# Optimization experiments

Measured on AMD Instinct MI355X. Metric: run time of the kernel, lower is better.

The kernel has to match this reference:

```python
import jax, jax.numpy as jnp
import numpy as np

EPS = 1e-6
MAX_TANH_ARG = 15.0


def setup_inputs() -> dict:
    key = jax.random.key(0)
    k1, k2, k3 = jax.random.split(key, 3)
    B, H, N, D = 2, 16, 2048, 64
    return {
        "q": jax.random.normal(k1, (B, H, N, D), dtype=jnp.float32),
        "k": jax.random.normal(k2, (B, H, N, D), dtype=jnp.float32),
        "v": jax.random.normal(k3, (B, H, N, D), dtype=jnp.float32),
        "c": jnp.ones((1,), dtype=jnp.float32),
        "beta": jnp.ones((1,), dtype=jnp.float32),
    }


def _exp_map(x, sqrt_c):
    # tangent space -> Poincare ball
    norm = jnp.maximum(jnp.linalg.norm(x, axis=-1, keepdims=True), EPS)
    tanh_arg = jnp.minimum(sqrt_c * norm, MAX_TANH_ARG)
    return x * (jnp.tanh(tanh_arg) / (sqrt_c * norm))


def reference(q, k, v, c, beta):
    # q, k, v: [B, H, N, D]; c, beta: [1] positive scalars
    causal, use_exp_map = True, True
    N = q.shape[2]
    c = jnp.maximum(c.astype(jnp.float32), EPS)  # [1]
    sqrt_c = jnp.sqrt(c)
    beta = beta.astype(jnp.float32)

    if use_exp_map:
        q_hyp = _exp_map(q, sqrt_c)
        k_hyp = _exp_map(k, sqrt_c)
    else:
        q_hyp, k_hyp = q, k

    q_n2 = jnp.sum(q_hyp * q_hyp, axis=-1, keepdims=True)          # [B,H,N,1]
    k_n2 = jnp.sum(k_hyp * k_hyp, axis=-1, keepdims=True)          # [B,H,N,1]
    qk = jnp.einsum('bhnd,bhmd->bhnm', q_hyp, k_hyp)               # [B,H,N,N]

    diff_n2 = jnp.maximum(q_n2 - 2.0 * qk + jnp.swapaxes(k_n2, -2, -1), 0.0)
    denom = jnp.maximum((1.0 - c * q_n2) * (1.0 - c * jnp.swapaxes(k_n2, -2, -1)), EPS)
    arg = jnp.maximum(1.0 + 2.0 * c * diff_n2 / denom, 1.0 + EPS)
    dist = jnp.arccosh(arg) / sqrt_c                               # Poincare distance
    scores = -beta * dist                                          # [B,H,N,N]

    if causal:
        mask = jnp.triu(jnp.ones((N, N), dtype=bool), k=1)
        scores = jnp.where(mask, -jnp.inf, scores)

    attn = jax.nn.softmax(scores, axis=-1)
    out = jnp.einsum('bhnm,bhmd->bhnd', attn, v)
    return out.astype(q.dtype)
```

## Files before the change

### kernel.cpp

```cpp
#include <hip/hip_runtime.h>
#include <hip/hip_bf16.h>

typedef __bf16 bf16x8 __attribute__((ext_vector_type(8)));
typedef float  f32x4  __attribute__((ext_vector_type(4)));

#define BDIM  2
#define HDIM  16
#define NDIM  2048
#define DDIM  64
#define BH    (BDIM*HDIM)
#define EPSF  1e-6f

__device__ __forceinline__ unsigned short f2bf(float x){
    union { float f; unsigned u; } a; a.f = x;
    unsigned r = a.u + 0x7fffu + ((a.u >> 16) & 1u);
    return (unsigned short)(r >> 16);
}

__global__ __launch_bounds__(256)
void prep_qk(const float* __restrict__ q, const float* __restrict__ k,
             unsigned short* __restrict__ qh, unsigned short* __restrict__ kh,
             float* __restrict__ qn2, float* __restrict__ kn2,
             const float* __restrict__ cp)
{
    const int tid = threadIdx.x;
    const int row = blockIdx.x * 16 + (tid >> 4);
    const int c0  = (tid & 15) * 4;
    const float c   = fmaxf(cp[0], EPSF);
    const float sqc = sqrtf(c);

    {
        float4 x = *(const float4*)(q + (size_t)row * DDIM + c0);
        float ss = fmaf(x.x, x.x, fmaf(x.y, x.y, fmaf(x.z, x.z, x.w * x.w)));
        #pragma unroll
        for (int off = 1; off < 16; off <<= 1) ss += __shfl_xor(ss, off);
        float sn    = fmaxf(sqrtf(ss), EPSF);
        float targ  = fminf(sqc * sn, 15.0f);
        float e     = exp2f(targ * 2.885390082f);
        float th    = (e - 1.0f) * __builtin_amdgcn_rcpf(e + 1.0f);
        float scale = th * __builtin_amdgcn_rcpf(sqc * sn);
        ushort4 o;
        o.x = f2bf(x.x * scale); o.y = f2bf(x.y * scale);
        o.z = f2bf(x.z * scale); o.w = f2bf(x.w * scale);
        *(ushort4*)(qh + (size_t)row * DDIM + c0) = o;
        if ((tid & 15) == 0) qn2[row] = ss * scale * scale;
    }
    {
        float4 x = *(const float4*)(k + (size_t)row * DDIM + c0);
        float ss = fmaf(x.x, x.x, fmaf(x.y, x.y, fmaf(x.z, x.z, x.w * x.w)));
        #pragma unroll
        for (int off = 1; off < 16; off <<= 1) ss += __shfl_xor(ss, off);
        float sn    = fmaxf(sqrtf(ss), EPSF);
        float targ  = fminf(sqc * sn, 15.0f);
        float e     = exp2f(targ * 2.885390082f);
        float th    = (e - 1.0f) * __builtin_amdgcn_rcpf(e + 1.0f);
        float scale = th * __builtin_amdgcn_rcpf(sqc * sn);
        ushort4 o;
        o.x = f2bf(x.x * scale); o.y = f2bf(x.y * scale);
        o.z = f2bf(x.z * scale); o.w = f2bf(x.w * scale);
        *(ushort4*)(kh + (size_t)row * DDIM + c0) = o;
        if ((tid & 15) == 0) kn2[row] = ss * scale * scale;
    }
}

__global__ __launch_bounds__(256)
void prep_v(const float* __restrict__ v, unsigned short* __restrict__ vt)
{
    __shared__ float t[64][65];
    const int bh = blockIdx.x >> 5;
    const int n0 = (blockIdx.x & 31) * 64;
    const int tid = threadIdx.x;

    #pragma unroll
    for (int i = 0; i < 4; ++i){
        int ch  = tid + i * 256;
        int row = ch >> 4;
        int c4  = ch & 15;
        const float4 g = *(const float4*)(v + ((size_t)bh * NDIM + n0 + row) * DDIM + c4 * 4);
        t[row][c4*4 + 0] = g.x; t[row][c4*4 + 1] = g.y;
        t[row][c4*4 + 2] = g.z; t[row][c4*4 + 3] = g.w;
    }
    __syncthreads();
    #pragma unroll
    for (int i = 0; i < 4; ++i){
        int ch = tid + i * 256;
        int d  = ch >> 4;
        int nc = ch & 15;
        size_t ob = ((size_t)bh * DDIM + d) * NDIM + n0 + nc * 4;
        #pragma unroll
        for (int j = 0; j < 4; ++j) vt[ob + j] = f2bf(t[nc*4 + j][d]);
    }
}

__global__ __launch_bounds__(256, 4)
void hyp_attn(const unsigned short* __restrict__ qh, const unsigned short* __restrict__ kh,
              const unsigned short* __restrict__ vtg,
              const float* __restrict__ qn2g, const float* __restrict__ kn2g,
              const float* __restrict__ cp, const float* __restrict__ bp,
              float* __restrict__ out)
{
    __shared__ unsigned short p_s[4][16 * 72];

    const int bh  = blockIdx.x;
    const int bg  = blockIdx.y;
    const int tid = threadIdx.x;
    const int ws  = tid >> 6;
    const int wv  = (ws + (bg >> 3)) & 3;
    const int l   = tid & 63;
    const int l15 = l & 15;
    const int lg  = l >> 4;

    const int j = (wv == 0) ? bg : (wv == 1) ? 127 - bg : (wv == 2) ? 63 - bg : 64 + bg;

    const float c   = fmaxf(cp[0], EPSF);
    const float sqc = sqrtf(c);
    const float nb2 = -bp[0] / sqc;
    const float tc  = 2.0f * c;

    const unsigned short* khb  = kh  + (size_t)bh * (NDIM * DDIM);
    const unsigned short* vtb  = vtg + (size_t)bh * (NDIM * DDIM);
    const float*          kn2b = kn2g + (size_t)bh * NDIM;

    const int q0 = j * 16;
    const size_t qbase = ((size_t)bh * NDIM + (q0 + l15)) * DDIM;
    const bf16x8 qa0 = *(const bf16x8*)(qh + qbase + lg * 8);
    const bf16x8 qa1 = *(const bf16x8*)(qh + qbase + 32 + lg * 8);

    const int qr0 = q0 + lg * 4;
    float qn2r[4], omq[4];
    #pragma unroll
    for (int r = 0; r < 4; ++r){
        qn2r[r] = qn2g[(size_t)bh * NDIM + qr0 + r];
        omq[r]  = 1.0f - c * qn2r[r];
    }

    float m2[4], lr[4];
    f32x4 O[4];
    #pragma unroll
    for (int r = 0; r < 4; ++r){ m2[r] = -1e30f; lr[r] = 0.0f; }
    #pragma unroll
    for (int vd = 0; vd < 4; ++vd) O[vd] = (f32x4){0.f, 0.f, 0.f, 0.f};

    unsigned short* pw = p_s[ws];
    const int ktend = j >> 2;

    for (int kt = 0; kt <= ktend; ++kt){
        const int k0 = kt * 64;

        float kn2m[4];
        #pragma unroll
        for (int f = 0; f < 4; ++f) kn2m[f] = kn2b[k0 + f * 16 + l15];

        f32x4 S[4];
        #pragma unroll
        for (int f = 0; f < 4; ++f){
            const unsigned short* kp = khb + (size_t)(k0 + f * 16 + l15) * DDIM + lg * 8;
            bf16x8 b0 = *(const bf16x8*)(kp);
            bf16x8 b1 = *(const bf16x8*)(kp + 32);
            f32x4 acc = (f32x4){0.f, 0.f, 0.f, 0.f};
            acc = __builtin_amdgcn_mfma_f32_16x16x32_bf16(qa0, b0, acc, 0, 0, 0);
            acc = __builtin_amdgcn_mfma_f32_16x16x32_bf16(qa1, b1, acc, 0, 0, 0);
            S[f] = acc;
        }

        bf16x8 vf[2][4];
        #pragma unroll
        for (int mc = 0; mc < 2; ++mc)
            #pragma unroll
            for (int vd = 0; vd < 4; ++vd)
                vf[mc][vd] = *(const bf16x8*)(vtb + (size_t)(vd * 16 + l15) * NDIM
                                              + k0 + mc * 32 + lg * 8);

        float sc[4][4], rmax[4];
        #pragma unroll
        for (int r = 0; r < 4; ++r) rmax[r] = -1e30f;
        #pragma unroll
        for (int f = 0; f < 4; ++f){
            const float kn2v = kn2m[f];
            const float omk  = 1.0f - c * kn2v;
            const int   m    = k0 + f * 16 + l15;
            #pragma unroll
            for (int r = 0; r < 4; ++r){
                float diff = fmaxf(fmaf(-2.0f, S[f][r], qn2r[r] + kn2v), 0.0f);
                float den  = fmaxf(omq[r] * omk, EPSF);
                float arg  = fmaxf(fmaf(tc * diff, __builtin_amdgcn_rcpf(den), 1.0f), 1.0f + EPSF);
                float w    = arg + sqrtf(fmaf(arg, arg, -1.0f));
                float s2   = nb2 * __log2f(w);
                s2 = (m > qr0 + r) ? -1e30f : s2;
                sc[f][r] = s2;
                rmax[r]  = fmaxf(rmax[r], s2);
            }
        }
        #pragma unroll
        for (int r = 0; r < 4; ++r){
            #pragma unroll
            for (int off = 1; off < 16; off <<= 1)
                rmax[r] = fmaxf(rmax[r], __shfl_xor(rmax[r], off));
        }
        bool up = (rmax[0] > m2[0]) | (rmax[1] > m2[1]) |
                  (rmax[2] > m2[2]) | (rmax[3] > m2[3]);
        if (__any(up)){
            #pragma unroll
            for (int r = 0; r < 4; ++r){
                float nm  = fmaxf(m2[r], rmax[r]);
                float scl = exp2f(m2[r] - nm);
                lr[r] *= scl; m2[r] = nm;
                #pragma unroll
                for (int vd = 0; vd < 4; ++vd) O[vd][r] *= scl;
            }
        }

        float psum[4] = {0.f, 0.f, 0.f, 0.f};
        #pragma unroll
        for (int f = 0; f < 4; ++f){
            const int fx = ((f ^ lg) << 4) + l15;
            #pragma unroll
            for (int r = 0; r < 4; ++r){
                float p = exp2f(sc[f][r] - m2[r]);
                psum[r] += p;
                pw[(lg * 4 + r) * 72 + fx] = f2bf(p);
            }
        }
        #pragma unroll
        for (int r = 0; r < 4; ++r){
            #pragma unroll
            for (int off = 1; off < 16; off <<= 1)
                psum[r] += __shfl_xor(psum[r], off);
            lr[r] += psum[r];
        }

        asm volatile("s_waitcnt lgkmcnt(0)" ::: "memory");

        #pragma unroll
        for (int mc = 0; mc < 2; ++mc){
            const int f  = 2 * mc + (lg >> 1);
            const int fx = f ^ ((l15 >> 2) & 3);
            bf16x8 pa = *(const bf16x8*)&pw[l15 * 72 + fx * 16 + (lg & 1) * 8];
            #pragma unroll
            for (int vd = 0; vd < 4; ++vd)
                O[vd] = __builtin_amdgcn_mfma_f32_16x16x32_bf16(pa, vf[mc][vd], O[vd], 0, 0, 0);
        }
    }

    #pragma unroll
    for (int r = 0; r < 4; ++r){
        float rl = __builtin_amdgcn_rcpf(lr[r]);
        #pragma unroll
        for (int vd = 0; vd < 4; ++vd)
            out[((size_t)bh * NDIM + qr0 + r) * DDIM + vd * 16 + l15] = O[vd][r] * rl;
    }
}

extern "C" void kernel_launch(void* const* d_in, const int* in_sizes, int n_in,
                              void* d_out, int out_size, void* d_ws, size_t ws_size,
                              hipStream_t stream)
{
    const float* q   = (const float*)d_in[0];
    const float* k   = (const float*)d_in[1];
    const float* v   = (const float*)d_in[2];
    const float* cp  = (const float*)d_in[3];
    const float* bp  = (const float*)d_in[4];
    float*       out = (float*)d_out;

    char* ws = (char*)d_ws;
    const size_t elems = (size_t)BH * NDIM * DDIM;
    unsigned short* qh  = (unsigned short*)ws;  ws += elems * 2;
    unsigned short* kh  = (unsigned short*)ws;  ws += elems * 2;
    unsigned short* vt  = (unsigned short*)ws;  ws += elems * 2;
    float*          qn2 = (float*)ws;           ws += (size_t)BH * NDIM * 4;
    float*          kn2 = (float*)ws;

    prep_qk<<<(BH * NDIM) / 16, 256, 0, stream>>>(q, k, qh, kh, qn2, kn2, cp);
    prep_v <<<BH * (NDIM / 64), 256, 0, stream>>>(v, vt);
    hyp_attn<<<dim3(BH, 32), 256, 0, stream>>>(qh, kh, vt, qn2, kn2, cp, bp, out);
}
```

Baseline: 276.6 us.

## Merge prep kernels, one-wave attention blocks, prefetch K tiles, mask only last tile

The two preprocessing kernels become one launch, and the V transpose now stores vectorised ushort4 writes. The attention kernel moves from 256-thread blocks covering four query tiles each to 64-thread single-wave blocks, one per query tile, with the longest rows launched first. K fragments and norms for the next tile are prefetched in registers while the current tile computes. The causal mask is applied only on the diagonal tile, and the clamp on diff at zero is dropped. This aims to cut launch overhead and hide global load latency, but adds register pressure, and removing the clamp could let a slightly negative squared distance from rounding through.

New measurement: 331.3 us. 19.8% more time.

```diff
diff --git a/kernel.cpp b/kernel.cpp
--- a/kernel.cpp
+++ b/kernel.cpp
@@ -1,5 +1,6 @@
 #include <hip/hip_runtime.h>
 #include <hip/hip_bf16.h>
+#include <type_traits>
 
 typedef __bf16 bf16x8 __attribute__((ext_vector_type(8)));
 typedef float  f32x4  __attribute__((ext_vector_type(4)));
@@ -11,6 +12,9 @@
 #define BH    (BDIM*HDIM)
 #define EPSF  1e-6f
 
+#define QK_BLOCKS (BH * NDIM / 16)
+#define V_BLOCKS  (BH * NDIM / 64)
+
 __device__ __forceinline__ unsigned short f2bf(float x){
     union { float f; unsigned u; } a; a.f = x;
     unsigned r = a.u + 0x7fffu + ((a.u >> 16) & 1u);
@@ -18,99 +22,96 @@
 }
 
 __global__ __launch_bounds__(256)
-void prep_qk(const float* __restrict__ q, const float* __restrict__ k,
-             unsigned short* __restrict__ qh, unsigned short* __restrict__ kh,
-             float* __restrict__ qn2, float* __restrict__ kn2,
-             const float* __restrict__ cp)
-{
-    const int tid = threadIdx.x;
-    const int row = blockIdx.x * 16 + (tid >> 4);
-    const int c0  = (tid & 15) * 4;
-    const float c   = fmaxf(cp[0], EPSF);
-    const float sqc = sqrtf(c);
-
-    {
-        float4 x = *(const float4*)(q + (size_t)row * DDIM + c0);
-        float ss = fmaf(x.x, x.x, fmaf(x.y, x.y, fmaf(x.z, x.z, x.w * x.w)));
-        #pragma unroll
-        for (int off = 1; off < 16; off <<= 1) ss += __shfl_xor(ss, off);
-        float sn    = fmaxf(sqrtf(ss), EPSF);
-        float targ  = fminf(sqc * sn, 15.0f);
-        float e     = exp2f(targ * 2.885390082f);
-        float th    = (e - 1.0f) * __builtin_amdgcn_rcpf(e + 1.0f);
-        float scale = th * __builtin_amdgcn_rcpf(sqc * sn);
-        ushort4 o;
-        o.x = f2bf(x.x * scale); o.y = f2bf(x.y * scale);
-        o.z = f2bf(x.z * scale); o.w = f2bf(x.w * scale);
-        *(ushort4*)(qh + (size_t)row * DDIM + c0) = o;
-        if ((tid & 15) == 0) qn2[row] = ss * scale * scale;
-    }
-    {
-        float4 x = *(const float4*)(k + (size_t)row * DDIM + c0);
-        float ss = fmaf(x.x, x.x, fmaf(x.y, x.y, fmaf(x.z, x.z, x.w * x.w)));
-        #pragma unroll
-        for (int off = 1; off < 16; off <<= 1) ss += __shfl_xor(ss, off);
-        float sn    = fmaxf(sqrtf(ss), EPSF);
-        float targ  = fminf(sqc * sn, 15.0f);
-        float e     = exp2f(targ * 2.885390082f);
-        float th    = (e - 1.0f) * __builtin_amdgcn_rcpf(e + 1.0f);
-        float scale = th * __builtin_amdgcn_rcpf(sqc * sn);
-        ushort4 o;
-        o.x = f2bf(x.x * scale); o.y = f2bf(x.y * scale);
-        o.z = f2bf(x.z * scale); o.w = f2bf(x.w * scale);
-        *(ushort4*)(kh + (size_t)row * DDIM + c0) = o;
-        if ((tid & 15) == 0) kn2[row] = ss * scale * scale;
-    }
-}
-
-__global__ __launch_bounds__(256)
-void prep_v(const float* __restrict__ v, unsigned short* __restrict__ vt)
+void prep(const float* __restrict__ q, const float* __restrict__ k,
+          const float* __restrict__ v,
+          unsigned short* __restrict__ qh, unsigned short* __restrict__ kh,
+          unsigned short* __restrict__ vt,
+          float* __restrict__ qn2, float* __restrict__ kn2,
+          const float* __restrict__ cp)
 {
     __shared__ float t[64][65];
-    const int bh = blockIdx.x >> 5;
-    const int n0 = (blockIdx.x & 31) * 64;
     const int tid = threadIdx.x;
 
-    #pragma unroll
-    for (int i = 0; i < 4; ++i){
-        int ch  = tid + i * 256;
-        int row = ch >> 4;
-        int c4  = ch & 15;
-        const float4 g = *(const float4*)(v + ((size_t)bh * NDIM + n0 + row) * DDIM + c4 * 4);
-        t[row][c4*4 + 0] = g.x; t[row][c4*4 + 1] = g.y;
-        t[row][c4*4 + 2] = g.z; t[row][c4*4 + 3] = g.w;
-    }
-    __syncthreads();
-    #pragma unroll
-    for (int i = 0; i < 4; ++i){
-        int ch = tid + i * 256;
-        int d  = ch >> 4;
-        int nc = ch & 15;
-        size_t ob = ((size_t)bh * DDIM + d) * NDIM + n0 + nc * 4;
-        #pragma unroll
-        for (int j = 0; j < 4; ++j) vt[ob + j] = f2bf(t[nc*4 + j][d]);
-    }
-}
-
-__global__ __launch_bounds__(256, 4)
+    if (blockIdx.x < QK_BLOCKS){
+        const int row = blockIdx.x * 16 + (tid >> 4);
+        const int c0  = (tid & 15) * 4;
+        const float c   = fmaxf(cp[0], EPSF);
+        const float sqc = sqrtf(c);
+
+        {
+            float4 x = *(const float4*)(q + (size_t)row * DDIM + c0);
+            float ss = fmaf(x.x, x.x, fmaf(x.y, x.y, fmaf(x.z, x.z, x.w * x.w)));
+            #pragma unroll
+            for (int off = 1; off < 16; off <<= 1) ss += __shfl_xor(ss, off);
+            float sn    = fmaxf(sqrtf(ss), EPSF);
+            float targ  = fminf(sqc * sn, 15.0f);
+            float e     = exp2f(targ * 2.885390082f);
+            float th    = (e - 1.0f) * __builtin_amdgcn_rcpf(e + 1.0f);
+            float scale = th * __builtin_amdgcn_rcpf(sqc * sn);
+            ushort4 o;
+            o.x = f2bf(x.x * scale); o.y = f2bf(x.y * scale);
+            o.z = f2bf(x.z * scale); o.w = f2bf(x.w * scale);
+            *(ushort4*)(qh + (size_t)row * DDIM + c0) = o;
+            if ((tid & 15) == 0) qn2[row] = ss * scale * scale;
+        }
+        {
+            float4 x = *(const float4*)(k + (size_t)row * DDIM + c0);
+            float ss = fmaf(x.x, x.x, fmaf(x.y, x.y, fmaf(x.z, x.z, x.w * x.w)));
+            #pragma unroll
+            for (int off = 1; off < 16; off <<= 1) ss += __shfl_xor(ss, off);
+            float sn    = fmaxf(sqrtf(ss), EPSF);
+            float targ  = fminf(sqc * sn, 15.0f);
+            float e     = exp2f(targ * 2.885390082f);
+            float th    = (e - 1.0f) * __builtin_amdgcn_rcpf(e + 1.0f);
+            float scale = th * __builtin_amdgcn_rcpf(sqc * sn);
+            ushort4 o;
+            o.x = f2bf(x.x * scale); o.y = f2bf(x.y * scale);
+            o.z = f2bf(x.z * scale); o.w = f2bf(x.w * scale);
+            *(ushort4*)(kh + (size_t)row * DDIM + c0) = o;
+            if ((tid & 15) == 0) kn2[row] = ss * scale * scale;
+        }
+    } else {
+        const int b  = blockIdx.x - QK_BLOCKS;
+        const int bh = b >> 5;
+        const int n0 = (b & 31) * 64;
+
+        #pragma unroll
+        for (int i = 0; i < 4; ++i){
+            int ch  = tid + i * 256;
+            int row = ch >> 4;
+            int c4  = ch & 15;
+            const float4 g = *(const float4*)(v + ((size_t)bh * NDIM + n0 + row) * DDIM + c4 * 4);
+            t[row][c4*4 + 0] = g.x; t[row][c4*4 + 1] = g.y;
+            t[row][c4*4 + 2] = g.z; t[row][c4*4 + 3] = g.w;
+        }
+        __syncthreads();
+        #pragma unroll
+        for (int i = 0; i < 4; ++i){
+            int ch = tid + i * 256;
+            int d  = ch >> 4;
+            int nc = ch & 15;
+            ushort4 o;
+            o.x = f2bf(t[nc*4 + 0][d]); o.y = f2bf(t[nc*4 + 1][d]);
+            o.z = f2bf(t[nc*4 + 2][d]); o.w = f2bf(t[nc*4 + 3][d]);
+            *(ushort4*)(vt + ((size_t)bh * DDIM + d) * NDIM + n0 + nc * 4) = o;
+        }
+    }
+}
+
+__global__ __launch_bounds__(64, 4)
 void hyp_attn(const unsigned short* __restrict__ qh, const unsigned short* __restrict__ kh,
               const unsigned short* __restrict__ vtg,
               const float* __restrict__ qn2g, const float* __restrict__ kn2g,
               const float* __restrict__ cp, const float* __restrict__ bp,
               float* __restrict__ out)
 {
-    __shared__ unsigned short p_s[4][16 * 72];
+    __shared__ unsigned short pw[16 * 72];
 
     const int bh  = blockIdx.x;
-    const int bg  = blockIdx.y;
-    const int tid = threadIdx.x;
-    const int ws  = tid >> 6;
-    const int wv  = (ws + (bg >> 3)) & 3;
-    const int l   = tid & 63;
+    const int j   = 127 - (int)blockIdx.y;
+    const int l   = threadIdx.x & 63;
     const int l15 = l & 15;
     const int lg  = l >> 4;
-
-    const int j = (wv == 0) ? bg : (wv == 1) ? 127 - bg : (wv == 2) ? 63 - bg : 64 + bg;
 
     const float c   = fmaxf(cp[0], EPSF);
     const float sqc = sqrtf(c);
@@ -141,28 +142,44 @@
     #pragma unroll
     for (int vd = 0; vd < 4; ++vd) O[vd] = (f32x4){0.f, 0.f, 0.f, 0.f};
 
-    unsigned short* pw = p_s[ws];
     const int ktend = j >> 2;
 
-    for (int kt = 0; kt <= ktend; ++kt){
+    bf16x8 kf0[4], kf1[4];
+    float  kn2n[4];
+    #pragma unroll
+    for (int f = 0; f < 4; ++f){
+        const unsigned short* kp = khb + (size_t)(f * 16 + l15) * DDIM + lg * 8;
+        kf0[f] = *(const bf16x8*)(kp);
+        kf1[f] = *(const bf16x8*)(kp + 32);
+        kn2n[f] = kn2b[f * 16 + l15];
+    }
+
+    auto tile_body = [&](int kt, auto MASKC){
+        constexpr bool MASK = decltype(MASKC)::value;
         const int k0 = kt * 64;
 
+        f32x4 S[4];
+        #pragma unroll
+        for (int f = 0; f < 4; ++f){
+            f32x4 acc = (f32x4){0.f, 0.f, 0.f, 0.f};
+            acc = __builtin_amdgcn_mfma_f32_16x16x32_bf16(qa0, kf0[f], acc, 0, 0, 0);
+            acc = __builtin_amdgcn_mfma_f32_16x16x32_bf16(qa1, kf1[f], acc, 0, 0, 0);
+            S[f] = acc;
+        }
         float kn2m[4];
         #pragma unroll
-        for (int f = 0; f < 4; ++f) kn2m[f] = kn2b[k0 + f * 16 + l15];
-
-        f32x4 S[4];
-        #pragma unroll
-        for (int f = 0; f < 4; ++f){
-            const unsigned short* kp = khb + (size_t)(k0 + f * 16 + l15) * DDIM + lg * 8;
-            bf16x8 b0 = *(const bf16x8*)(kp);
-            bf16x8 b1 = *(const bf16x8*)(kp + 32);
-            f32x4 acc = (f32x4){0.f, 0.f, 0.f, 0.f};
-            acc = __builtin_amdgcn_mfma_f32_16x16x32_bf16(qa0, b0, acc, 0, 0, 0);
-            acc = __builtin_amdgcn_mfma_f32_16x16x32_bf16(qa1, b1, acc, 0, 0, 0);
-            S[f] = acc;
-        }
-
+        for (int f = 0; f < 4; ++f) kn2m[f] = kn2n[f];
+
+        if (kt < ktend){
+            const int k0n = k0 + 64;
+            #pragma unroll
+            for (int f = 0; f < 4; ++f){
+                const unsigned short* kp = khb + (size_t)(k0n + f * 16 + l15) * DDIM + lg * 8;
+                kf0[f] = *(const bf16x8*)(kp);
+                kf1[f] = *(const bf16x8*)(kp + 32);
+                kn2n[f] = kn2b[k0n + f * 16 + l15];
+            }
+        }
         bf16x8 vf[2][4];
         #pragma unroll
         for (int mc = 0; mc < 2; ++mc)
@@ -178,15 +195,14 @@
         for (int f = 0; f < 4; ++f){
             const float kn2v = kn2m[f];
             const float omk  = 1.0f - c * kn2v;
-            const int   m    = k0 + f * 16 + l15;
             #pragma unroll
             for (int r = 0; r < 4; ++r){
-                float diff = fmaxf(fmaf(-2.0f, S[f][r], qn2r[r] + kn2v), 0.0f);
+                float diff = fmaf(-2.0f, S[f][r], qn2r[r] + kn2v);
                 float den  = fmaxf(omq[r] * omk, EPSF);
                 float arg  = fmaxf(fmaf(tc * diff, __builtin_amdgcn_rcpf(den), 1.0f), 1.0f + EPSF);
                 float w    = arg + sqrtf(fmaf(arg, arg, -1.0f));
                 float s2   = nb2 * __log2f(w);
-                s2 = (m > qr0 + r) ? -1e30f : s2;
+                if (MASK) s2 = (k0 + f * 16 + l15 > qr0 + r) ? -1e30f : s2;
                 sc[f][r] = s2;
                 rmax[r]  = fmaxf(rmax[r], s2);
             }
@@ -240,7 +256,10 @@
             for (int vd = 0; vd < 4; ++vd)
                 O[vd] = __builtin_amdgcn_mfma_f32_16x16x32_bf16(pa, vf[mc][vd], O[vd], 0, 0, 0);
         }
-    }
+    };
+
+    for (int kt = 0; kt < ktend; ++kt) tile_body(kt, std::bool_constant<false>{});
+    tile_body(ktend, std::bool_constant<true>{});
 
     #pragma unroll
     for (int r = 0; r < 4; ++r){
@@ -270,7 +289,6 @@
     float*          qn2 = (float*)ws;           ws += (size_t)BH * NDIM * 4;
     float*          kn2 = (float*)ws;
 
-    prep_qk<<<(BH * NDIM) / 16, 256, 0, stream>>>(q, k, qh, kh, qn2, kn2, cp);
-    prep_v <<<BH * (NDIM / 64), 256, 0, stream>>>(v, vt);
-    hyp_attn<<<dim3(BH, 32), 256, 0, stream>>>(qh, kh, vt, qn2, kn2, cp, bp, out);
-}
+    prep<<<QK_BLOCKS + V_BLOCKS, 256, 0, stream>>>(q, k, v, qh, kh, vt, qn2, kn2, cp);
+    hyp_attn<<<dim3(BH, 128), 64, 0, stream>>>(qh, kh, vt, qn2, kn2, cp, bp, out);
+}
```
